# Kernel tuning notes

Hardware: AMD Instinct MI355X
Metric: run time of the kernel (lower is better)

## Reference

```python
import jax, jax.numpy as jnp
import numpy as np

B, S, E, H = 4, 4096, 1024, 16
D = E // H  # head_dim = 64
EPS = 1e-6


def setup_inputs() -> dict:
    key = jax.random.key(0)
    ks = jax.random.split(key, 11)
    inv = 1.0 / np.sqrt(E)
    return {
        "query": jax.random.normal(ks[0], (B, S, E), dtype=jnp.float32),
        "key": jax.random.normal(ks[1], (B, S, E), dtype=jnp.float32),
        "value": jax.random.normal(ks[2], (B, S, E), dtype=jnp.float32),
        "key_padding_mask": jnp.zeros((B, S), dtype=bool),
        "Wq": jax.random.uniform(ks[3], (E, E), jnp.float32, -inv, inv),
        "bq": jnp.zeros((E,), jnp.float32),
        "Wk": jax.random.uniform(ks[4], (E, E), jnp.float32, -inv, inv),
        "bk": jnp.zeros((E,), jnp.float32),
        "Wv": jax.random.uniform(ks[5], (E, E), jnp.float32, -inv, inv),
        "bv": jnp.zeros((E,), jnp.float32),
        "Wo": jax.random.uniform(ks[6], (E, E), jnp.float32, -inv, inv),
        "bo": jnp.zeros((E,), jnp.float32),
    }


def _heads(x):
    # (B,S,E) -> (B,H,S,D)
    return x.reshape(B, -1, H, D).transpose(0, 2, 1, 3)


def reference(query, key, value, key_padding_mask, Wq, bq, Wk, bk, Wv, bv, Wo, bo):
    q = _heads(query @ Wq.T + bq)
    k = _heads(key @ Wk.T + bk)
    v = _heads(value @ Wv.T + bv)

    q_aug = jax.nn.relu(q) + EPS
    k_aug = jax.nn.relu(k) + EPS
    # mask out padded keys: (B,S_k) -> (B,1,S_k,1)
    k_aug = jnp.where(key_padding_mask[:, None, :, None], 0.0, k_aug)

    kv_context = jnp.einsum("bhsd,bhsv->bhdv", k_aug, v)  # (B,H,D,D)
    k_sum = k_aug.sum(axis=2)                                # (B,H,D)
    denom = jnp.einsum("bhqd,bhd->bhq", q_aug, k_sum)
    denom = jnp.maximum(denom, EPS)

    attn = jnp.einsum("bhqd,bhdv->bhqv", q_aug, kv_context) / denom[..., None]
    attn = attn.transpose(0, 2, 1, 3).reshape(B, -1, E)      # (B,S_q,E)
    # dropout is identity in eval mode
    return attn @ Wo.T + bo
```

## Files before the change

kernel.cpp:

```cpp
#include <hip/hip_runtime.h>
#include <hip/hip_bf16.h>
#include <stdint.h>

#define B_ 4
#define S_ 4096
#define E_ 1024
#define H_ 16
#define D_ 64
#define M_ (B_*S_)
constexpr float kEPS = 1e-6f;

typedef unsigned short u16;
typedef unsigned char  u8;
typedef __bf16 bf16x8 __attribute__((ext_vector_type(8)));
typedef float  f32x4  __attribute__((ext_vector_type(4)));
typedef u16    u16x8  __attribute__((ext_vector_type(8)));

typedef const __attribute__((address_space(1))) void* gaddr_t;
typedef __attribute__((address_space(3))) void*       laddr_t;

__device__ __forceinline__ u16 f2bf(float f) {
    union { float f; uint32_t u; } v; v.f = f;
    uint32_t u = v.u;
    u += 0x7fffu + ((u >> 16) & 1u);
    return (u16)(u >> 16);
}
__device__ __forceinline__ float hi2f(uint32_t d) {
    union { uint32_t u; float f; } v; v.u = d & 0xffff0000u;
    return v.f;
}
__device__ __forceinline__ float lo2f(uint32_t d) {
    union { uint32_t u; float f; } v; v.u = d << 16;
    return v.f;
}

#define VM_WAIT(n) asm volatile("s_waitcnt vmcnt(" #n ")" ::: "memory")
#define LG0        asm volatile("s_waitcnt lgkmcnt(0)" ::: "memory")
#define SBAR       asm volatile("s_barrier" ::: "memory")

__global__ __launch_bounds__(256)
void cvt3_kernel(const float* __restrict__ s0, const float* __restrict__ s1,
                 const float* __restrict__ s2,
                 u16* __restrict__ d0, u16* __restrict__ d1, u16* __restrict__ d2,
                 int n4)
{
    const int z = blockIdx.y;
    const float* src = (z == 0) ? s0 : (z == 1) ? s1 : s2;
    u16*         dst = (z == 0) ? d0 : (z == 1) ? d1 : d2;
    const int stride = gridDim.x * blockDim.x;
    for (int i = blockIdx.x * blockDim.x + threadIdx.x; i < n4; i += stride) {
        float4 v = reinterpret_cast<const float4*>(src)[i];
        ushort4 o;
        o.x = f2bf(v.x); o.y = f2bf(v.y); o.z = f2bf(v.z); o.w = f2bf(v.w);
        reinterpret_cast<ushort4*>(dst)[i] = o;
    }
}

__global__ __launch_bounds__(256)
void cvtw_kernel(const float* __restrict__ w0, const float* __restrict__ w1,
                 const float* __restrict__ w2, const float* __restrict__ w3,
                 u16* __restrict__ o0, u16* __restrict__ o1,
                 u16* __restrict__ o2, u16* __restrict__ o3)
{
    const int z = blockIdx.y;
    const float* src = (z == 0) ? w0 : (z == 1) ? w1 : (z == 2) ? w2 : w3;
    u16*         dst = (z == 0) ? o0 : (z == 1) ? o1 : (z == 2) ? o2 : o3;
    const int i = blockIdx.x * blockDim.x + threadIdx.x;
    float4 v = reinterpret_cast<const float4*>(src)[i];
    ushort4 o;
    o.x = f2bf(v.x); o.y = f2bf(v.y); o.z = f2bf(v.z); o.w = f2bf(v.w);
    reinterpret_cast<ushort4*>(dst)[i] = o;
}

#define BM 256
#define BN 256
#define BKT 64
#define NKT (E_/BKT)

struct QKVArgs {
    const u16*   A[3];
    const u16*   W[3];
    const float* bias[3];
    const u8*    mask;
    u16*         C[3];
};

template<bool MERGED>
__global__ __launch_bounds__(512, 2)
void gemm8(QKVArgs qa,
           const u16* __restrict__ A1, const u16* __restrict__ Bw1,
           const float* __restrict__ bias1, float* __restrict__ Cf)
{
    extern __shared__ u16 lds[];
    const int tid  = threadIdx.x;
    const int wid  = tid >> 6, lane = tid & 63;
    const int wqr  = wid >> 2, wqc = wid & 3;
    const int m0   = blockIdx.x * BM;
    const int n0   = blockIdx.y * BN;
    const int fr   = lane & 15;
    const int cg   = lane >> 4;

    const u16* A;  const u16* Bw;  const float* bias;  u16* Cb;  int epi;
    if constexpr (MERGED) {
        const int z = blockIdx.z;
        A = qa.A[z]; Bw = qa.W[z]; bias = qa.bias[z]; Cb = qa.C[z]; epi = z + 1;
    } else {
        A = A1; Bw = Bw1; bias = bias1; Cb = nullptr; epi = 0;
    }

    const int srow = tid >> 3;
    const int ssc  = tid & 7;
    const int sck  = ssc ^ (srow & 7);
    const u16* aS = A  + (size_t)(m0 + srow)*E_ + sck*8;
    const u16* bS = Bw + (size_t)(n0 + srow)*E_ + sck*8;
    const int sd0 = tid*8, sd1 = (tid + 512)*8;

    int arow[4], brow[2];
#pragma unroll
    for (int mf = 0; mf < 4; ++mf) arow[mf] = (wqr*64 + mf*16 + fr) * 64;
#pragma unroll
    for (int nf = 0; nf < 2; ++nf) brow[nf] = (wqc*32 + nf*16 + fr) * 64;
    const int kx0 = ((cg)     ^ (fr & 7)) * 8;
    const int kx1 = ((4 + cg) ^ (fr & 7)) * 8;

    f32x4 acc[2][2][4][2] = {};
    bf16x8 afr[4][2];

    float bias_v[2][2];
#pragma unroll
    for (int nh = 0; nh < 2; ++nh)
#pragma unroll
        for (int nf = 0; nf < 2; ++nf)
            bias_v[nh][nf] = bias[n0 + nh*128 + wqc*32 + nf*16 + fr];

#define STAGE(BUF, MAT, HH, T) do { \
        u16* dst_ = lds + (BUF)*32768 + (MAT)*16384 + (HH)*8192; \
        const u16* src_ = ((MAT) ? bS : aS) + (size_t)(HH)*128*E_ + (size_t)(T)*BKT; \
        __builtin_amdgcn_global_load_lds((gaddr_t)(src_),                  (laddr_t)(dst_ + sd0), 16, 0, 0); \
        __builtin_amdgcn_global_load_lds((gaddr_t)(src_ + (size_t)64*E_), (laddr_t)(dst_ + sd1), 16, 0, 0); \
    } while (0)

#define PH(BUF, MH, NH, STG_STMT, WAIT_STMT) do { \
        const u16* Ab_ = lds + (BUF)*32768 + (MH)*8192; \
        const u16* Bb_ = lds + (BUF)*32768 + 16384 + (NH)*8192; \
        if ((NH) == 0) { \
            _Pragma("unroll") \
            for (int mf_ = 0; mf_ < 4; ++mf_) { \
                afr[mf_][0] = *reinterpret_cast<const bf16x8*>(Ab_ + arow[mf_] + kx0); \
                afr[mf_][1] = *reinterpret_cast<const bf16x8*>(Ab_ + arow[mf_] + kx1); \
            } \
        } \
        bf16x8 bfv[2][2]; \
        _Pragma("unroll") \
        for (int nf_ = 0; nf_ < 2; ++nf_) { \
            bfv[nf_][0] = *reinterpret_cast<const bf16x8*>(Bb_ + brow[nf_] + kx0); \
            bfv[nf_][1] = *reinterpret_cast<const bf16x8*>(Bb_ + brow[nf_] + kx1); \
        } \
        STG_STMT; \
        WAIT_STMT; \
        SBAR; \
        LG0; \
        __builtin_amdgcn_sched_barrier(0); \
        __builtin_amdgcn_s_setprio(1); \
        _Pragma("unroll") \
        for (int mf_ = 0; mf_ < 4; ++mf_) { \
            _Pragma("unroll") \
            for (int nf_ = 0; nf_ < 2; ++nf_) { \
                acc[MH][NH][mf_][nf_] = __builtin_amdgcn_mfma_f32_16x16x32_bf16(afr[mf_][0], bfv[nf_][0], acc[MH][NH][mf_][nf_], 0, 0, 0); \
                acc[MH][NH][mf_][nf_] = __builtin_amdgcn_mfma_f32_16x16x32_bf16(afr[mf_][1], bfv[nf_][1], acc[MH][NH][mf_][nf_], 0, 0, 0); \
            } \
        } \
        __builtin_amdgcn_s_setprio(0); \
        SBAR; \
    } while (0)

    STAGE(0, 0, 0, 0);
    STAGE(0, 1, 0, 0);
    STAGE(0, 0, 1, 0);
    STAGE(0, 1, 1, 0);
    STAGE(1, 0, 0, 1);
    STAGE(1, 1, 0, 1);
    VM_WAIT(4);
    SBAR;
    __builtin_amdgcn_sched_barrier(0);

#pragma unroll 1
    for (int i = 0; i < 7; ++i) {
        const int T1 = 2*i + 1, T2 = 2*i + 2, T3 = 2*i + 3;
        PH(0, 0, 0, STAGE(1, 0, 1, T1), ;);
        PH(0, 0, 1, STAGE(1, 1, 1, T1), ;);
        PH(0, 1, 0, STAGE(0, 0, 0, T2), ;);
        PH(0, 1, 1, STAGE(0, 1, 0, T2), VM_WAIT(4));
        PH(1, 0, 0, STAGE(0, 0, 1, T2), ;);
        PH(1, 0, 1, STAGE(0, 1, 1, T2), ;);
        PH(1, 1, 0, STAGE(1, 0, 0, T3), ;);
        PH(1, 1, 1, STAGE(1, 1, 0, T3), VM_WAIT(4));
    }
    PH(0, 0, 0, STAGE(1, 0, 1, 15), ;);
    PH(0, 0, 1, STAGE(1, 1, 1, 15), ;);
    PH(0, 1, 0, ;, ;);
    PH(0, 1, 1, ;, VM_WAIT(0));
    PH(1, 0, 0, ;, ;);
    PH(1, 0, 1, ;, ;);
    PH(1, 1, 0, ;, ;);
    PH(1, 1, 1, ;, ;);
#undef PH
#undef STAGE

    const int bblk = m0 >> 12;
    const int sloc = m0 & 4095;
#pragma unroll
    for (int mh = 0; mh < 2; ++mh) {
#pragma unroll
    for (int nh = 0; nh < 2; ++nh) {
#pragma unroll
    for (int mf = 0; mf < 4; ++mf) {
#pragma unroll
        for (int nf = 0; nf < 2; ++nf) {
            const int gn = n0 + nh*128 + wqc*32 + nf*16 + fr;
            const int mb = mh*128 + wqr*64 + mf*16 + cg*4;
            if (epi >= 2) {
                ushort4 o;
#pragma unroll
                for (int r = 0; r < 4; ++r) {
                    float x = acc[mh][nh][mf][nf][r] + bias_v[nh][nf];
                    if (epi == 2) {
                        x = fmaxf(x, 0.f) + kEPS;
                        if (qa.mask[m0 + mb + r]) x = 0.f;
                    }
                    ((u16*)&o)[r] = f2bf(x);
                }
                *reinterpret_cast<ushort4*>(Cb + ((size_t)(bblk*1024 + gn))*4096 + sloc + mb) = o;
            } else if (epi == 1) {
#pragma unroll
                for (int r = 0; r < 4; ++r) {
                    const int gm = m0 + mb + r;
                    float x = acc[mh][nh][mf][nf][r] + bias_v[nh][nf];
                    x = fmaxf(x, 0.f) + kEPS;
                    Cb[(size_t)gm*E_ + gn] = f2bf(x);
                }
            } else {
#pragma unroll
                for (int r = 0; r < 4; ++r) {
                    const int gm = m0 + mb + r;
                    Cf[(size_t)gm*E_ + gn] = acc[mh][nh][mf][nf][r] + bias_v[nh][nf];
                }
            }
        }
    }
    }
    }
}

#define NSC 8
#define KCH (S_/NSC)
__global__ __launch_bounds__(256)
void kv_mfma_kernel(const u16* __restrict__ KaT, const u16* __restrict__ VvT,
                    float* __restrict__ kvp, float* __restrict__ ksp)
{
    __shared__ float sm[4][64];
    const int bh = blockIdx.x, sc = blockIdx.y;
    const int tid = threadIdx.x;
    const int w = tid >> 6, lane = tid & 63;
    const int fr = lane & 15, cg = lane >> 4;

    const u16* Ar = VvT + ((size_t)bh*64 + w*16 + fr)*4096 + sc*KCH;
    const u16* Br0 = KaT + ((size_t)bh*64 + fr)*4096 + sc*KCH;

    f32x4 acc[4] = {};
#pragma unroll 2
    for (int ks = 0; ks < KCH/32; ++ks) {
        const int ko = ks*32 + cg*8;
        bf16x8 af = *reinterpret_cast<const bf16x8*>(Ar + ko);
#pragma unroll
        for (int nf = 0; nf < 4; ++nf) {
            bf16x8 bf = *reinterpret_cast<const bf16x8*>(Br0 + (size_t)nf*16*4096 + ko);
            acc[nf] = __builtin_amdgcn_mfma_f32_16x16x32_bf16(af, bf, acc[nf], 0, 0, 0);
        }
    }
    float* dst = kvp + ((size_t)sc*64 + bh)*4096;
#pragma unroll
    for (int nf = 0; nf < 4; ++nf)
#pragma unroll
        for (int r = 0; r < 4; ++r)
            dst[(w*16 + cg*4 + r)*64 + nf*16 + fr] = acc[nf][r];

    {
        const int d = tid & 63, qq = tid >> 6;
        const u16* kr = KaT + ((size_t)bh*64 + d)*4096 + sc*KCH + qq*(KCH/4);
        float s = 0.f;
#pragma unroll 4
        for (int i = 0; i < KCH/4/8; ++i) {
            bf16x8 kk = *reinterpret_cast<const bf16x8*>(kr + i*8);
#pragma unroll
            for (int j = 0; j < 8; ++j) s += (float)kk[j];
        }
        sm[qq][d] = s;
    }
    __syncthreads();
    if (tid < 64)
        ksp[((size_t)sc*64 + bh)*64 + tid] = sm[0][tid] + sm[1][tid] + sm[2][tid] + sm[3][tid];
}

__global__ __launch_bounds__(256)
void kv_reduce_kernel(const float* __restrict__ kvp, const float* __restrict__ ksp,
                      u16* __restrict__ kvT, float* __restrict__ ksum)
{
    const int i = blockIdx.x*256 + threadIdx.x;
    float s = 0.f;
#pragma unroll
    for (int c = 0; c < NSC; ++c) s += kvp[(size_t)c*262144 + i];
    kvT[i] = f2bf(s);
    if (i < 4096) {
        float t = 0.f;
#pragma unroll
        for (int c = 0; c < NSC; ++c) t += ksp[(size_t)c*4096 + i];
        ksum[i] = t;
    }
}

__global__ __launch_bounds__(256)
void attn_kernel(const u16* __restrict__ Qa, const u16* __restrict__ kvT,
                 const float* __restrict__ ksum, u16* __restrict__ attn)
{
    __shared__ u16  Qs[256*64];
    __shared__ u16  Ts[64*64];
    __shared__ float kss[64];
    __shared__ float invd[256];

    const int bh = blockIdx.x, b = bh >> 4, h = bh & 15;
    const int s0 = blockIdx.y * 256;
    const int tid = threadIdx.x;
    const int wid = tid >> 6, lane = tid & 63;
    const int fr = lane & 15, cg = lane >> 4;

#pragma unroll
    for (int j = 0; j < 8; ++j) {
        int L = (wid*8 + j)*64 + lane;
        int row = L >> 3, c = L & 7;
        int cs = c ^ (row & 7);
        const u16* src = Qa + (size_t)(b*S_ + s0 + row)*E_ + h*64 + cs*8;
        __builtin_amdgcn_global_load_lds((gaddr_t)src, (laddr_t)(Qs + L*8), 16, 0, 0);
    }
#pragma unroll
    for (int k = 0; k < 2; ++k) {
        int g = k*256 + tid;
        int v = g >> 3, c = g & 7;
        uint4 q = *reinterpret_cast<const uint4*>(kvT + (size_t)bh*4096 + g*8);
        int cs = c ^ (v & 7);
        *reinterpret_cast<uint4*>(Ts + v*64 + cs*8) = q;
    }
    if (tid < 64) kss[tid] = ksum[bh*64 + tid];
    asm volatile("s_waitcnt vmcnt(0) lgkmcnt(0)" ::: "memory");
    __syncthreads();

    {
        float den = 0.f;
#pragma unroll
        for (int c = 0; c < 8; ++c) {
            uint4 qc = *reinterpret_cast<const uint4*>(Qs + tid*64 + (c ^ (tid & 7))*8);
            den += lo2f(qc.x)*kss[c*8+0] + hi2f(qc.x)*kss[c*8+1]
                 + lo2f(qc.y)*kss[c*8+2] + hi2f(qc.y)*kss[c*8+3]
                 + lo2f(qc.z)*kss[c*8+4] + hi2f(qc.z)*kss[c*8+5]
                 + lo2f(qc.w)*kss[c*8+6] + hi2f(qc.w)*kss[c*8+7];
        }
        invd[tid] = 1.0f / fmaxf(den, kEPS);
    }
    __syncthreads();

    f32x4 acc[4][4] = {};
#pragma unroll
    for (int ks = 0; ks < 2; ++ks) {
        bf16x8 bfrag[4];
#pragma unroll
        for (int nf = 0; nf < 4; ++nf) {
            int v = nf*16 + fr;
            bfrag[nf] = *reinterpret_cast<const bf16x8*>(Ts + v*64 + ((ks*4 + cg) ^ (v & 7))*8);
        }
#pragma unroll
        for (int mf = 0; mf < 4; ++mf) {
            int m = wid*64 + mf*16 + fr;
            bf16x8 afrag = *reinterpret_cast<const bf16x8*>(Qs + m*64 + ((ks*4 + cg) ^ (m & 7))*8);
#pragma unroll
            for (int nf = 0; nf < 4; ++nf)
                acc[mf][nf] = __builtin_amdgcn_mfma_f32_16x16x32_bf16(afrag, bfrag[nf], acc[mf][nf], 0, 0, 0);
        }
    }

#pragma unroll
    for (int mf = 0; mf < 4; ++mf) {
#pragma unroll
        for (int nf = 0; nf < 4; ++nf) {
            const int v = nf*16 + fr;
#pragma unroll
            for (int r = 0; r < 4; ++r) {
                const int row = wid*64 + mf*16 + cg*4 + r;
                float x = acc[mf][nf][r] * invd[row];
                attn[(size_t)(b*S_ + s0 + row)*E_ + h*64 + v] = f2bf(x);
            }
        }
    }
}

extern "C" void kernel_launch(void* const* d_in, const int* in_sizes, int n_in,
                              void* d_out, int out_size, void* d_ws, size_t ws_size,
                              hipStream_t stream)
{
    const float* query = (const float*)d_in[0];
    const float* key   = (const float*)d_in[1];
    const float* value = (const float*)d_in[2];
    const u8*    mask  = (const u8*)d_in[3];
    const float* Wq = (const float*)d_in[4];
    const float* bq = (const float*)d_in[5];
    const float* Wk = (const float*)d_in[6];
    const float* bk = (const float*)d_in[7];
    const float* Wv = (const float*)d_in[8];
    const float* bv = (const float*)d_in[9];
    const float* Wo = (const float*)d_in[10];
    const float* bo = (const float*)d_in[11];
    float* out = (float*)d_out;

    const size_t SZ_ME = (size_t)M_ * E_;
    const size_t SZ_EE = (size_t)E_ * E_;

    char* ws = (char*)d_ws;
    u16* qx   = (u16*)ws; ws += SZ_ME*2;
    u16* kx   = (u16*)ws; ws += SZ_ME*2;
    u16* vx   = (u16*)ws; ws += SZ_ME*2;
    u16* Qa   = (u16*)ws; ws += SZ_ME*2;
    u16* KaT  = (u16*)ws; ws += SZ_ME*2;
    u16* VvT  = (u16*)ws; ws += SZ_ME*2;
    u16* wqb  = (u16*)ws; ws += SZ_EE*2;
    u16* wkb  = (u16*)ws; ws += SZ_EE*2;
    u16* wvb  = (u16*)ws; ws += SZ_EE*2;
    u16* wob  = (u16*)ws; ws += SZ_EE*2;
    float* kvp = (float*)ws; ws += (size_t)NSC*64*4096*4;
    float* ksp = (float*)ws; ws += (size_t)NSC*4096*4;
    u16*  kvT  = (u16*)ws;  ws += (size_t)64*4096*2;
    float* ksum= (float*)ws; ws += 4096*4;

    u16* attnb = qx;

    cvt3_kernel<<<dim3(2048, 3), 256, 0, stream>>>(query, key, value, qx, kx, vx, (int)(SZ_ME/4));
    cvtw_kernel<<<dim3(1024, 4), 256, 0, stream>>>(Wq, Wk, Wv, Wo, wqb, wkb, wvb, wob);

    QKVArgs qa;
    qa.A[0] = qx;  qa.A[1] = kx;  qa.A[2] = vx;
    qa.W[0] = wqb; qa.W[1] = wkb; qa.W[2] = wvb;
    qa.bias[0] = bq; qa.bias[1] = bk; qa.bias[2] = bv;
    qa.mask = mask;
    qa.C[0] = Qa; qa.C[1] = KaT; qa.C[2] = VvT;
    dim3 ggrid(M_/BM, E_/BN, 3);
    constexpr size_t LDS_BYTES = 2 * 32768 * sizeof(u16);
    gemm8<true><<<ggrid, 512, LDS_BYTES, stream>>>(qa, nullptr, nullptr, nullptr, nullptr);

    kv_mfma_kernel<<<dim3(64, NSC), 256, 0, stream>>>(KaT, VvT, kvp, ksp);
    kv_reduce_kernel<<<1024, 256, 0, stream>>>(kvp, ksp, kvT, ksum);

    attn_kernel<<<dim3(B_*H_, S_/256), 256, 0, stream>>>(Qa, kvT, ksum, attnb);

    QKVArgs dummy = {};
    dummy.mask = mask;
    gemm8<false><<<dim3(M_/BM, E_/BN, 1), 512, LDS_BYTES, stream>>>(dummy, attnb, wob, bo, out);
}
```

Baseline: 263.8 us.

## Reuse B fragments across M halves and deepen GEMM prefetch to full stage

The GEMM main loop now keeps two B-fragment register sets and loads B from LDS only once per N-half, reusing it across both M-halves, which cuts LDS reads. The stage ordering and vmcnt waits are reworked so a full next K-tile is prefetched with finer-grained waits that allow more global loads in flight. This adds register pressure and makes the wait counts delicate, so a miscount could create a race or a stall.

```diff
diff --git a/kernel.cpp b/kernel.cpp
--- a/kernel.cpp
+++ b/kernel.cpp
@@ -125,6 +125,7 @@
 
     f32x4 acc[2][2][4][2] = {};
     bf16x8 afr[4][2];
+    bf16x8 bfr0[2][2], bfr1[2][2];
 
     float bias_v[2][2];
 #pragma unroll
@@ -140,21 +141,22 @@
         __builtin_amdgcn_global_load_lds((gaddr_t)(src_ + (size_t)64*E_), (laddr_t)(dst_ + sd1), 16, 0, 0); \
     } while (0)
 
-#define PH(BUF, MH, NH, STG_STMT, WAIT_STMT) do { \
-        const u16* Ab_ = lds + (BUF)*32768 + (MH)*8192; \
-        const u16* Bb_ = lds + (BUF)*32768 + 16384 + (NH)*8192; \
-        if ((NH) == 0) { \
+#define PH(BUF, MH, NH, BFRX, LOADA, LOADB, STG_STMT, WAIT_STMT) do { \
+        if (LOADA) { \
+            const u16* Ab_ = lds + (BUF)*32768 + (MH)*8192; \
             _Pragma("unroll") \
             for (int mf_ = 0; mf_ < 4; ++mf_) { \
                 afr[mf_][0] = *reinterpret_cast<const bf16x8*>(Ab_ + arow[mf_] + kx0); \
                 afr[mf_][1] = *reinterpret_cast<const bf16x8*>(Ab_ + arow[mf_] + kx1); \
             } \
         } \
-        bf16x8 bfv[2][2]; \
-        _Pragma("unroll") \
-        for (int nf_ = 0; nf_ < 2; ++nf_) { \
-            bfv[nf_][0] = *reinterpret_cast<const bf16x8*>(Bb_ + brow[nf_] + kx0); \
-            bfv[nf_][1] = *reinterpret_cast<const bf16x8*>(Bb_ + brow[nf_] + kx1); \
+        if (LOADB) { \
+            const u16* Bb_ = lds + (BUF)*32768 + 16384 + (NH)*8192; \
+            _Pragma("unroll") \
+            for (int nf_ = 0; nf_ < 2; ++nf_) { \
+                BFRX[nf_][0] = *reinterpret_cast<const bf16x8*>(Bb_ + brow[nf_] + kx0); \
+                BFRX[nf_][1] = *reinterpret_cast<const bf16x8*>(Bb_ + brow[nf_] + kx1); \
+            } \
         } \
         STG_STMT; \
         WAIT_STMT; \
@@ -166,44 +168,44 @@
         for (int mf_ = 0; mf_ < 4; ++mf_) { \
             _Pragma("unroll") \
             for (int nf_ = 0; nf_ < 2; ++nf_) { \
-                acc[MH][NH][mf_][nf_] = __builtin_amdgcn_mfma_f32_16x16x32_bf16(afr[mf_][0], bfv[nf_][0], acc[MH][NH][mf_][nf_], 0, 0, 0); \
-                acc[MH][NH][mf_][nf_] = __builtin_amdgcn_mfma_f32_16x16x32_bf16(afr[mf_][1], bfv[nf_][1], acc[MH][NH][mf_][nf_], 0, 0, 0); \
+                acc[MH][NH][mf_][nf_] = __builtin_amdgcn_mfma_f32_16x16x32_bf16(afr[mf_][0], BFRX[nf_][0], acc[MH][NH][mf_][nf_], 0, 0, 0); \
+                acc[MH][NH][mf_][nf_] = __builtin_amdgcn_mfma_f32_16x16x32_bf16(afr[mf_][1], BFRX[nf_][1], acc[MH][NH][mf_][nf_], 0, 0, 0); \
             } \
         } \
         __builtin_amdgcn_s_setprio(0); \
         SBAR; \
     } while (0)
 
-    STAGE(0, 0, 0, 0);
-    STAGE(0, 1, 0, 0);
+    STAGE(0, 0, 0, 0); STAGE(0, 1, 0, 0);
+    STAGE(0, 1, 1, 0);
     STAGE(0, 0, 1, 0);
-    STAGE(0, 1, 1, 0);
-    STAGE(1, 0, 0, 1);
-    STAGE(1, 1, 0, 1);
-    VM_WAIT(4);
+    STAGE(1, 0, 0, 1); STAGE(1, 1, 0, 1);
+    STAGE(1, 1, 1, 1);
+    STAGE(1, 0, 1, 1);
+    VM_WAIT(8);
     SBAR;
     __builtin_amdgcn_sched_barrier(0);
 
 #pragma unroll 1
     for (int i = 0; i < 7; ++i) {
-        const int T1 = 2*i + 1, T2 = 2*i + 2, T3 = 2*i + 3;
-        PH(0, 0, 0, STAGE(1, 0, 1, T1), ;);
-        PH(0, 0, 1, STAGE(1, 1, 1, T1), ;);
-        PH(0, 1, 0, STAGE(0, 0, 0, T2), ;);
-        PH(0, 1, 1, STAGE(0, 1, 0, T2), VM_WAIT(4));
-        PH(1, 0, 0, STAGE(0, 0, 1, T2), ;);
-        PH(1, 0, 1, STAGE(0, 1, 1, T2), ;);
-        PH(1, 1, 0, STAGE(1, 0, 0, T3), ;);
-        PH(1, 1, 1, STAGE(1, 1, 0, T3), VM_WAIT(4));
-    }
-    PH(0, 0, 0, STAGE(1, 0, 1, 15), ;);
-    PH(0, 0, 1, STAGE(1, 1, 1, 15), ;);
-    PH(0, 1, 0, ;, ;);
-    PH(0, 1, 1, ;, VM_WAIT(0));
-    PH(1, 0, 0, ;, ;);
-    PH(1, 0, 1, ;, ;);
-    PH(1, 1, 0, ;, ;);
-    PH(1, 1, 1, ;, ;);
+        const int T2 = 2*i + 2, T3 = 2*i + 3;
+        PH(0, 0, 0, bfr0, 1, 1, ;,                                        VM_WAIT(10));
+        PH(0, 0, 1, bfr1, 0, 1, { STAGE(0,0,0,T2); STAGE(0,1,0,T2); },    VM_WAIT(12));
+        PH(0, 1, 0, bfr0, 1, 0, STAGE(0,1,1,T2),                          ;);
+        PH(0, 1, 1, bfr1, 0, 0, STAGE(0,0,1,T2),                          VM_WAIT(12));
+        PH(1, 0, 0, bfr0, 1, 1, ;,                                        VM_WAIT(10));
+        PH(1, 0, 1, bfr1, 0, 1, { STAGE(1,0,0,T3); STAGE(1,1,0,T3); },    VM_WAIT(12));
+        PH(1, 1, 0, bfr0, 1, 0, STAGE(1,1,1,T3),                          ;);
+        PH(1, 1, 1, bfr1, 0, 0, STAGE(1,0,1,T3),                          VM_WAIT(12));
+    }
+    PH(0, 0, 0, bfr0, 1, 1, ;, VM_WAIT(10));
+    PH(0, 0, 1, bfr1, 0, 1, ;, VM_WAIT(8));
+    PH(0, 1, 0, bfr0, 1, 0, ;, ;);
+    PH(0, 1, 1, bfr1, 0, 0, ;, VM_WAIT(4));
+    PH(1, 0, 0, bfr0, 1, 1, ;, VM_WAIT(2));
+    PH(1, 0, 1, bfr1, 0, 1, ;, VM_WAIT(0));
+    PH(1, 1, 0, bfr0, 1, 0, ;, ;);
+    PH(1, 1, 1, bfr1, 0, 0, ;, ;);
 #undef PH
 #undef STAGE
 
```

After: 261.5 us, median of 2. Within noise of the previous version (-0.9%).

## Replace 256x256 eight-phase GEMM with simpler 256x128 double-buffered kernel

Applied to the files above, without the earlier changes.

The hand-scheduled 256x256x64 GEMM with its eight-phase quarter-tile pipeline is replaced by a 256x128 tile with K-step 32 and a plain double-buffered loop that prefetches the next K slice while issuing MFMAs on the current one. The LDS footprint drops, and launch bounds now ask for four blocks per CU, aiming at higher occupancy and more blocks in the grid. In exchange, each tile reuses its operands less and takes a full barrier plus vmcnt(0) wait on every K step, so more global/L2 traffic and more synchronisation overhead are exposed. The LDS swizzle is rewritten for the 32-wide K slice.

```diff
diff --git a/kernel.cpp b/kernel.cpp
--- a/kernel.cpp
+++ b/kernel.cpp
@@ -72,10 +72,10 @@
     reinterpret_cast<ushort4*>(dst)[i] = o;
 }
 
-#define BM 256
-#define BN 256
-#define BKT 64
-#define NKT (E_/BKT)
+#define BM2 256
+#define BN2 128
+#define BKT2 32
+#define NT2 (E_/BKT2)
 
 struct QKVArgs {
     const u16*   A[3];
@@ -86,17 +86,17 @@
 };
 
 template<bool MERGED>
-__global__ __launch_bounds__(512, 2)
-void gemm8(QKVArgs qa,
-           const u16* __restrict__ A1, const u16* __restrict__ Bw1,
-           const float* __restrict__ bias1, float* __restrict__ Cf)
+__global__ __launch_bounds__(512, 4)
+void gemm2b(QKVArgs qa,
+            const u16* __restrict__ A1, const u16* __restrict__ Bw1,
+            const float* __restrict__ bias1, float* __restrict__ Cf)
 {
     extern __shared__ u16 lds[];
     const int tid  = threadIdx.x;
     const int wid  = tid >> 6, lane = tid & 63;
-    const int wqr  = wid >> 2, wqc = wid & 3;
-    const int m0   = blockIdx.x * BM;
-    const int n0   = blockIdx.y * BN;
+    const int wqr  = wid >> 1, wqc = wid & 1;
+    const int m0   = blockIdx.x * BM2;
+    const int n0   = blockIdx.y * BN2;
     const int fr   = lane & 15;
     const int cg   = lane >> 4;
 
@@ -108,122 +108,78 @@
         A = A1; Bw = Bw1; bias = bias1; Cb = nullptr; epi = 0;
     }
 
-    const int srow = tid >> 3;
-    const int ssc  = tid & 7;
-    const int sck  = ssc ^ (srow & 7);
-    const u16* aS = A  + (size_t)(m0 + srow)*E_ + sck*8;
-    const u16* bS = Bw + (size_t)(n0 + srow)*E_ + sck*8;
-    const int sd0 = tid*8, sd1 = (tid + 512)*8;
-
-    int arow[4], brow[2];
-#pragma unroll
-    for (int mf = 0; mf < 4; ++mf) arow[mf] = (wqr*64 + mf*16 + fr) * 64;
-#pragma unroll
-    for (int nf = 0; nf < 2; ++nf) brow[nf] = (wqc*32 + nf*16 + fr) * 64;
-    const int kx0 = ((cg)     ^ (fr & 7)) * 8;
-    const int kx1 = ((4 + cg) ^ (fr & 7)) * 8;
-
-    f32x4 acc[2][2][4][2] = {};
-    bf16x8 afr[4][2];
-
-    float bias_v[2][2];
-#pragma unroll
-    for (int nh = 0; nh < 2; ++nh)
-#pragma unroll
-        for (int nf = 0; nf < 2; ++nf)
-            bias_v[nh][nf] = bias[n0 + nh*128 + wqc*32 + nf*16 + fr];
-
-#define STAGE(BUF, MAT, HH, T) do { \
-        u16* dst_ = lds + (BUF)*32768 + (MAT)*16384 + (HH)*8192; \
-        const u16* src_ = ((MAT) ? bS : aS) + (size_t)(HH)*128*E_ + (size_t)(T)*BKT; \
-        __builtin_amdgcn_global_load_lds((gaddr_t)(src_),                  (laddr_t)(dst_ + sd0), 16, 0, 0); \
-        __builtin_amdgcn_global_load_lds((gaddr_t)(src_ + (size_t)64*E_), (laddr_t)(dst_ + sd1), 16, 0, 0); \
+    const int srow = tid >> 2;
+    const int skey = (srow ^ (srow >> 2)) & 3;
+    const int sck  = (tid & 3) ^ skey;
+    const u16* aS0 = A  + (size_t)(m0 + srow)*E_        + sck*8;
+    const u16* aS1 = A  + (size_t)(m0 + 128 + srow)*E_  + sck*8;
+    const u16* bS0 = Bw + (size_t)(n0 + srow)*E_        + sck*8;
+
+    const int lkey = (fr ^ (fr >> 2)) & 3;
+    const int kxr  = (cg ^ lkey) * 8;
+    int arow[4], brow[4];
+#pragma unroll
+    for (int mf = 0; mf < 4; ++mf) arow[mf] = (wqr*64 + mf*16 + fr)*32 + kxr;
+#pragma unroll
+    for (int nf = 0; nf < 4; ++nf) brow[nf] = 8192 + (wqc*64 + nf*16 + fr)*32 + kxr;
+
+    f32x4 acc[4][4] = {};
+
+    float bias_v[4];
+#pragma unroll
+    for (int nf = 0; nf < 4; ++nf) bias_v[nf] = bias[n0 + wqc*64 + nf*16 + fr];
+
+#define STAGE(BUF, T) do { \
+        const size_t ko_ = (size_t)(T) * BKT2; \
+        u16* ab_ = lds + (BUF)*12288; \
+        __builtin_amdgcn_global_load_lds((gaddr_t)(aS0 + ko_), (laddr_t)(ab_ + tid*8),          16, 0, 0); \
+        __builtin_amdgcn_global_load_lds((gaddr_t)(aS1 + ko_), (laddr_t)(ab_ + (tid+512)*8),    16, 0, 0); \
+        __builtin_amdgcn_global_load_lds((gaddr_t)(bS0 + ko_), (laddr_t)(ab_ + 8192 + tid*8),   16, 0, 0); \
     } while (0)
 
-#define PH(BUF, MH, NH, STG_STMT, WAIT_STMT) do { \
-        const u16* Ab_ = lds + (BUF)*32768 + (MH)*8192; \
-        const u16* Bb_ = lds + (BUF)*32768 + 16384 + (NH)*8192; \
-        if ((NH) == 0) { \
-            _Pragma("unroll") \
-            for (int mf_ = 0; mf_ < 4; ++mf_) { \
-                afr[mf_][0] = *reinterpret_cast<const bf16x8*>(Ab_ + arow[mf_] + kx0); \
-                afr[mf_][1] = *reinterpret_cast<const bf16x8*>(Ab_ + arow[mf_] + kx1); \
-            } \
-        } \
-        bf16x8 bfv[2][2]; \
-        _Pragma("unroll") \
-        for (int nf_ = 0; nf_ < 2; ++nf_) { \
-            bfv[nf_][0] = *reinterpret_cast<const bf16x8*>(Bb_ + brow[nf_] + kx0); \
-            bfv[nf_][1] = *reinterpret_cast<const bf16x8*>(Bb_ + brow[nf_] + kx1); \
-        } \
-        STG_STMT; \
-        WAIT_STMT; \
-        SBAR; \
-        LG0; \
-        __builtin_amdgcn_sched_barrier(0); \
-        __builtin_amdgcn_s_setprio(1); \
-        _Pragma("unroll") \
-        for (int mf_ = 0; mf_ < 4; ++mf_) { \
-            _Pragma("unroll") \
-            for (int nf_ = 0; nf_ < 2; ++nf_) { \
-                acc[MH][NH][mf_][nf_] = __builtin_amdgcn_mfma_f32_16x16x32_bf16(afr[mf_][0], bfv[nf_][0], acc[MH][NH][mf_][nf_], 0, 0, 0); \
-                acc[MH][NH][mf_][nf_] = __builtin_amdgcn_mfma_f32_16x16x32_bf16(afr[mf_][1], bfv[nf_][1], acc[MH][NH][mf_][nf_], 0, 0, 0); \
-            } \
-        } \
-        __builtin_amdgcn_s_setprio(0); \
-        SBAR; \
-    } while (0)
-
-    STAGE(0, 0, 0, 0);
-    STAGE(0, 1, 0, 0);
-    STAGE(0, 0, 1, 0);
-    STAGE(0, 1, 1, 0);
-    STAGE(1, 0, 0, 1);
-    STAGE(1, 1, 0, 1);
-    VM_WAIT(4);
+    STAGE(0, 0);
+    VM_WAIT(0);
     SBAR;
     __builtin_amdgcn_sched_barrier(0);
 
 #pragma unroll 1
-    for (int i = 0; i < 7; ++i) {
-        const int T1 = 2*i + 1, T2 = 2*i + 2, T3 = 2*i + 3;
-        PH(0, 0, 0, STAGE(1, 0, 1, T1), ;);
-        PH(0, 0, 1, STAGE(1, 1, 1, T1), ;);
-        PH(0, 1, 0, STAGE(0, 0, 0, T2), ;);
-        PH(0, 1, 1, STAGE(0, 1, 0, T2), VM_WAIT(4));
-        PH(1, 0, 0, STAGE(0, 0, 1, T2), ;);
-        PH(1, 0, 1, STAGE(0, 1, 1, T2), ;);
-        PH(1, 1, 0, STAGE(1, 0, 0, T3), ;);
-        PH(1, 1, 1, STAGE(1, 1, 0, T3), VM_WAIT(4));
-    }
-    PH(0, 0, 0, STAGE(1, 0, 1, 15), ;);
-    PH(0, 0, 1, STAGE(1, 1, 1, 15), ;);
-    PH(0, 1, 0, ;, ;);
-    PH(0, 1, 1, ;, VM_WAIT(0));
-    PH(1, 0, 0, ;, ;);
-    PH(1, 0, 1, ;, ;);
-    PH(1, 1, 0, ;, ;);
-    PH(1, 1, 1, ;, ;);
-#undef PH
+    for (int T = 0; T < NT2; ++T) {
+        const int cb = T & 1;
+        const u16* buf = lds + cb*12288;
+        bf16x8 afr[4], bfv[4];
+#pragma unroll
+        for (int mf = 0; mf < 4; ++mf) afr[mf] = *reinterpret_cast<const bf16x8*>(buf + arow[mf]);
+#pragma unroll
+        for (int nf = 0; nf < 4; ++nf) bfv[nf] = *reinterpret_cast<const bf16x8*>(buf + brow[nf]);
+        if (T < NT2 - 1) STAGE(cb ^ 1, T + 1);
+        LG0;
+        __builtin_amdgcn_sched_barrier(0);
+        __builtin_amdgcn_s_setprio(1);
+#pragma unroll
+        for (int mf = 0; mf < 4; ++mf)
+#pragma unroll
+            for (int nf = 0; nf < 4; ++nf)
+                acc[mf][nf] = __builtin_amdgcn_mfma_f32_16x16x32_bf16(afr[mf], bfv[nf], acc[mf][nf], 0, 0, 0);
+        __builtin_amdgcn_s_setprio(0);
+        VM_WAIT(0);
+        SBAR;
+        __builtin_amdgcn_sched_barrier(0);
+    }
 #undef STAGE
 
     const int bblk = m0 >> 12;
     const int sloc = m0 & 4095;
 #pragma unroll
-    for (int mh = 0; mh < 2; ++mh) {
-#pragma unroll
-    for (int nh = 0; nh < 2; ++nh) {
-#pragma unroll
     for (int mf = 0; mf < 4; ++mf) {
 #pragma unroll
-        for (int nf = 0; nf < 2; ++nf) {
-            const int gn = n0 + nh*128 + wqc*32 + nf*16 + fr;
-            const int mb = mh*128 + wqr*64 + mf*16 + cg*4;
+        for (int nf = 0; nf < 4; ++nf) {
+            const int gn = n0 + wqc*64 + nf*16 + fr;
+            const int mb = wqr*64 + mf*16 + cg*4;
             if (epi >= 2) {
                 ushort4 o;
 #pragma unroll
                 for (int r = 0; r < 4; ++r) {
-                    float x = acc[mh][nh][mf][nf][r] + bias_v[nh][nf];
+                    float x = acc[mf][nf][r] + bias_v[nf];
                     if (epi == 2) {
                         x = fmaxf(x, 0.f) + kEPS;
                         if (qa.mask[m0 + mb + r]) x = 0.f;
@@ -235,7 +191,7 @@
 #pragma unroll
                 for (int r = 0; r < 4; ++r) {
                     const int gm = m0 + mb + r;
-                    float x = acc[mh][nh][mf][nf][r] + bias_v[nh][nf];
+                    float x = acc[mf][nf][r] + bias_v[nf];
                     x = fmaxf(x, 0.f) + kEPS;
                     Cb[(size_t)gm*E_ + gn] = f2bf(x);
                 }
@@ -243,12 +199,10 @@
 #pragma unroll
                 for (int r = 0; r < 4; ++r) {
                     const int gm = m0 + mb + r;
-                    Cf[(size_t)gm*E_ + gn] = acc[mh][nh][mf][nf][r] + bias_v[nh][nf];
+                    Cf[(size_t)gm*E_ + gn] = acc[mf][nf][r] + bias_v[nf];
                 }
             }
         }
-    }
-    }
     }
 }
 
@@ -450,9 +404,9 @@
     qa.bias[0] = bq; qa.bias[1] = bk; qa.bias[2] = bv;
     qa.mask = mask;
     qa.C[0] = Qa; qa.C[1] = KaT; qa.C[2] = VvT;
-    dim3 ggrid(M_/BM, E_/BN, 3);
-    constexpr size_t LDS_BYTES = 2 * 32768 * sizeof(u16);
-    gemm8<true><<<ggrid, 512, LDS_BYTES, stream>>>(qa, nullptr, nullptr, nullptr, nullptr);
+    dim3 ggrid(M_/BM2, E_/BN2, 3);
+    constexpr size_t LDS_BYTES = 2 * 12288 * sizeof(u16);
+    gemm2b<true><<<ggrid, 512, LDS_BYTES, stream>>>(qa, nullptr, nullptr, nullptr, nullptr);
 
     kv_mfma_kernel<<<dim3(64, NSC), 256, 0, stream>>>(KaT, VvT, kvp, ksp);
     kv_reduce_kernel<<<1024, 256, 0, stream>>>(kvp, ksp, kvT, ksum);
@@ -461,5 +415,5 @@
 
     QKVArgs dummy = {};
     dummy.mask = mask;
-    gemm8<false><<<dim3(M_/BM, E_/BN, 1), 512, LDS_BYTES, stream>>>(dummy, attnb, wob, bo, out);
-}
+    gemm2b<false><<<dim3(M_/BM2, E_/BN2, 1), 512, LDS_BYTES, stream>>>(dummy, attnb, wob, bo, out);
+}
```

Measured after the change: 279.9 us. 1.06x slower.

## Make QKV GEMM persistent over three projections with cross-GEMM prefetch

Applied to the files above, without the earlier changes.

Replaces the z-dimension grid of three projection GEMMs with a single block that processes Q, K and V sequentially for the same tile. The next projection's first k-tiles are staged into LDS during the tail of the current one, so pipeline fill and epilogue overlap across projections. This also removes the wave-quantization tail of the larger grid and preloads mask bytes as packed words. In exchange the grid launches only one block per CU, so occupancy is halved, and register pressure rises from holding three bias sets.

```diff
diff --git a/kernel.cpp b/kernel.cpp
--- a/kernel.cpp
+++ b/kernel.cpp
@@ -85,11 +85,11 @@
     u16*         C[3];
 };
 
-template<bool MERGED>
+template<int NZ>
 __global__ __launch_bounds__(512, 2)
-void gemm8(QKVArgs qa,
-           const u16* __restrict__ A1, const u16* __restrict__ Bw1,
-           const float* __restrict__ bias1, float* __restrict__ Cf)
+void gemm8z(QKVArgs qa,
+            const u16* __restrict__ A1, const u16* __restrict__ Bw1,
+            const float* __restrict__ bias1, float* __restrict__ Cf)
 {
     extern __shared__ u16 lds[];
     const int tid  = threadIdx.x;
@@ -100,19 +100,11 @@
     const int fr   = lane & 15;
     const int cg   = lane >> 4;
 
-    const u16* A;  const u16* Bw;  const float* bias;  u16* Cb;  int epi;
-    if constexpr (MERGED) {
-        const int z = blockIdx.z;
-        A = qa.A[z]; Bw = qa.W[z]; bias = qa.bias[z]; Cb = qa.C[z]; epi = z + 1;
-    } else {
-        A = A1; Bw = Bw1; bias = bias1; Cb = nullptr; epi = 0;
-    }
-
     const int srow = tid >> 3;
     const int ssc  = tid & 7;
     const int sck  = ssc ^ (srow & 7);
-    const u16* aS = A  + (size_t)(m0 + srow)*E_ + sck*8;
-    const u16* bS = Bw + (size_t)(n0 + srow)*E_ + sck*8;
+    const size_t aofs = (size_t)(m0 + srow)*E_ + sck*8;
+    const size_t bofs = (size_t)(n0 + srow)*E_ + sck*8;
     const int sd0 = tid*8, sd1 = (tid + 512)*8;
 
     int arow[4], brow[2];
@@ -126,19 +118,40 @@
     f32x4 acc[2][2][4][2] = {};
     bf16x8 afr[4][2];
 
-    float bias_v[2][2];
-#pragma unroll
-    for (int nh = 0; nh < 2; ++nh)
-#pragma unroll
-        for (int nf = 0; nf < 2; ++nf)
-            bias_v[nh][nf] = bias[n0 + nh*128 + wqc*32 + nf*16 + fr];
-
-#define STAGE(BUF, MAT, HH, T) do { \
+    float ba[NZ][2][2];
+#pragma unroll
+    for (int j = 0; j < NZ; ++j) {
+        const float* bp = (NZ == 3)
+            ? ((j == 0) ? qa.bias[0] : (j == 1) ? qa.bias[1] : qa.bias[2])
+            : bias1;
+#pragma unroll
+        for (int nh = 0; nh < 2; ++nh)
+#pragma unroll
+            for (int nf = 0; nf < 2; ++nf)
+                ba[j][nh][nf] = bp[n0 + nh*128 + wqc*32 + nf*16 + fr];
+    }
+    uint32_t mask_w[8] = {};
+    if constexpr (NZ == 3) {
+#pragma unroll
+        for (int mh = 0; mh < 2; ++mh)
+#pragma unroll
+            for (int mf = 0; mf < 4; ++mf)
+                mask_w[mh*4+mf] = *reinterpret_cast<const uint32_t*>(
+                    qa.mask + m0 + mh*128 + wqr*64 + mf*16 + cg*4);
+    }
+
+    const u16* Acur = (NZ == 3) ? qa.A[0] : A1;
+    const u16* Bcur = (NZ == 3) ? qa.W[0] : Bw1;
+
+#define STG(AP, BP, BUF, MAT, HH, T) do { \
         u16* dst_ = lds + (BUF)*32768 + (MAT)*16384 + (HH)*8192; \
-        const u16* src_ = ((MAT) ? bS : aS) + (size_t)(HH)*128*E_ + (size_t)(T)*BKT; \
+        const u16* src_ = ((MAT) ? ((BP) + bofs) : ((AP) + aofs)) \
+                          + (size_t)(HH)*128*E_ + (size_t)(T)*BKT; \
         __builtin_amdgcn_global_load_lds((gaddr_t)(src_),                  (laddr_t)(dst_ + sd0), 16, 0, 0); \
         __builtin_amdgcn_global_load_lds((gaddr_t)(src_ + (size_t)64*E_), (laddr_t)(dst_ + sd1), 16, 0, 0); \
     } while (0)
+#define STAGE(BUF, MAT, HH, T)  STG(Acur,  Bcur,  BUF, MAT, HH, T)
+#define STAGEN(BUF, MAT, HH, T) STG(Anext, Bnext, BUF, MAT, HH, T)
 
 #define PH(BUF, MH, NH, STG_STMT, WAIT_STMT) do { \
         const u16* Ab_ = lds + (BUF)*32768 + (MH)*8192; \
@@ -185,71 +198,121 @@
     __builtin_amdgcn_sched_barrier(0);
 
 #pragma unroll 1
-    for (int i = 0; i < 7; ++i) {
-        const int T1 = 2*i + 1, T2 = 2*i + 2, T3 = 2*i + 3;
-        PH(0, 0, 0, STAGE(1, 0, 1, T1), ;);
-        PH(0, 0, 1, STAGE(1, 1, 1, T1), ;);
-        PH(0, 1, 0, STAGE(0, 0, 0, T2), ;);
-        PH(0, 1, 1, STAGE(0, 1, 0, T2), VM_WAIT(4));
-        PH(1, 0, 0, STAGE(0, 0, 1, T2), ;);
-        PH(1, 0, 1, STAGE(0, 1, 1, T2), ;);
-        PH(1, 1, 0, STAGE(1, 0, 0, T3), ;);
-        PH(1, 1, 1, STAGE(1, 1, 0, T3), VM_WAIT(4));
-    }
-    PH(0, 0, 0, STAGE(1, 0, 1, 15), ;);
-    PH(0, 0, 1, STAGE(1, 1, 1, 15), ;);
-    PH(0, 1, 0, ;, ;);
-    PH(0, 1, 1, ;, VM_WAIT(0));
-    PH(1, 0, 0, ;, ;);
-    PH(1, 0, 1, ;, ;);
-    PH(1, 1, 0, ;, ;);
-    PH(1, 1, 1, ;, ;);
+    for (int z = 0; z < NZ; ++z) {
+        const u16* Anext = Acur;
+        const u16* Bnext = Bcur;
+        if constexpr (NZ == 3) {
+            Anext = (z == 0) ? qa.A[1] : qa.A[2];
+            Bnext = (z == 0) ? qa.W[1] : qa.W[2];
+        }
+
+#pragma unroll 1
+        for (int i = 0; i < 7; ++i) {
+            const int T1 = 2*i + 1, T2 = 2*i + 2, T3 = 2*i + 3;
+            PH(0, 0, 0, STAGE(1, 0, 1, T1), ;);
+            PH(0, 0, 1, STAGE(1, 1, 1, T1), ;);
+            PH(0, 1, 0, STAGE(0, 0, 0, T2), ;);
+            PH(0, 1, 1, STAGE(0, 1, 0, T2), VM_WAIT(4));
+            PH(1, 0, 0, STAGE(0, 0, 1, T2), ;);
+            PH(1, 0, 1, STAGE(0, 1, 1, T2), ;);
+            PH(1, 1, 0, STAGE(1, 0, 0, T3), ;);
+            PH(1, 1, 1, STAGE(1, 1, 0, T3), VM_WAIT(4));
+        }
+        if (z < NZ - 1) {
+            PH(0, 0, 0, STAGE(1, 0, 1, 15), ;);
+            PH(0, 0, 1, STAGE(1, 1, 1, 15), ;);
+            PH(0, 1, 0, STAGEN(0, 0, 0, 0), ;);
+            PH(0, 1, 1, STAGEN(0, 1, 0, 0), VM_WAIT(4));
+            PH(1, 0, 0, STAGEN(0, 0, 1, 0), ;);
+            PH(1, 0, 1, STAGEN(0, 1, 1, 0), ;);
+            PH(1, 1, 0, STAGEN(1, 0, 0, 1), ;);
+            PH(1, 1, 1, STAGEN(1, 1, 0, 1), VM_WAIT(4));
+        } else {
+            PH(0, 0, 0, STAGE(1, 0, 1, 15), ;);
+            PH(0, 0, 1, STAGE(1, 1, 1, 15), ;);
+            PH(0, 1, 0, ;, ;);
+            PH(0, 1, 1, ;, VM_WAIT(0));
+            PH(1, 0, 0, ;, ;);
+            PH(1, 0, 1, ;, ;);
+            PH(1, 1, 0, ;, ;);
+            PH(1, 1, 1, ;, ;);
+        }
+
+        const int epi = (NZ == 3) ? z + 1 : 0;
+        u16* Cb = nullptr;
+        if constexpr (NZ == 3)
+            Cb = (z == 0) ? qa.C[0] : (z == 1) ? qa.C[1] : qa.C[2];
+        float bcur[2][2];
+#pragma unroll
+        for (int nh = 0; nh < 2; ++nh)
+#pragma unroll
+            for (int nf = 0; nf < 2; ++nf)
+                bcur[nh][nf] = (NZ == 1 || z == 0) ? ba[0][nh][nf]
+                             : (NZ == 3 && z == 1) ? ba[NZ > 1 ? 1 : 0][nh][nf]
+                                                   : ba[NZ > 2 ? 2 : 0][nh][nf];
+
+        const int bblk = m0 >> 12;
+        const int sloc = m0 & 4095;
+#pragma unroll
+        for (int mh = 0; mh < 2; ++mh) {
+#pragma unroll
+        for (int nh = 0; nh < 2; ++nh) {
+#pragma unroll
+        for (int mf = 0; mf < 4; ++mf) {
+#pragma unroll
+            for (int nf = 0; nf < 2; ++nf) {
+                const int gn = n0 + nh*128 + wqc*32 + nf*16 + fr;
+                const int mb = mh*128 + wqr*64 + mf*16 + cg*4;
+                if (epi >= 2) {
+                    ushort4 o;
+#pragma unroll
+                    for (int r = 0; r < 4; ++r) {
+                        float x = acc[mh][nh][mf][nf][r] + bcur[nh][nf];
+                        if (epi == 2) {
+                            x = fmaxf(x, 0.f) + kEPS;
+                            if ((mask_w[mh*4+mf] >> (r*8)) & 0xffu) x = 0.f;
+                        }
+                        ((u16*)&o)[r] = f2bf(x);
+                    }
+                    *reinterpret_cast<ushort4*>(Cb + ((size_t)(bblk*1024 + gn))*4096 + sloc + mb) = o;
+                } else if (epi == 1) {
+#pragma unroll
+                    for (int r = 0; r < 4; ++r) {
+                        const int gm = m0 + mb + r;
+                        float x = acc[mh][nh][mf][nf][r] + bcur[nh][nf];
+                        x = fmaxf(x, 0.f) + kEPS;
+                        Cb[(size_t)gm*E_ + gn] = f2bf(x);
+                    }
+                } else {
+#pragma unroll
+                    for (int r = 0; r < 4; ++r) {
+                        const int gm = m0 + mb + r;
+                        Cf[(size_t)gm*E_ + gn] = acc[mh][nh][mf][nf][r] + bcur[nh][nf];
+                    }
+                }
+            }
+        }
+        }
+        }
+
+        if (z < NZ - 1) {
+#pragma unroll
+            for (int a = 0; a < 2; ++a)
+#pragma unroll
+            for (int b = 0; b < 2; ++b)
+#pragma unroll
+            for (int c = 0; c < 4; ++c)
+#pragma unroll
+            for (int d = 0; d < 2; ++d)
+                acc[a][b][c][d] = f32x4{0.f, 0.f, 0.f, 0.f};
+            Acur = Anext;
+            Bcur = Bnext;
+        }
+    }
 #undef PH
 #undef STAGE
-
-    const int bblk = m0 >> 12;
-    const int sloc = m0 & 4095;
-#pragma unroll
-    for (int mh = 0; mh < 2; ++mh) {
-#pragma unroll
-    for (int nh = 0; nh < 2; ++nh) {
-#pragma unroll
-    for (int mf = 0; mf < 4; ++mf) {
-#pragma unroll
-        for (int nf = 0; nf < 2; ++nf) {
-            const int gn = n0 + nh*128 + wqc*32 + nf*16 + fr;
-            const int mb = mh*128 + wqr*64 + mf*16 + cg*4;
-            if (epi >= 2) {
-                ushort4 o;
-#pragma unroll
-                for (int r = 0; r < 4; ++r) {
-                    float x = acc[mh][nh][mf][nf][r] + bias_v[nh][nf];
-                    if (epi == 2) {
-                        x = fmaxf(x, 0.f) + kEPS;
-                        if (qa.mask[m0 + mb + r]) x = 0.f;
-                    }
-                    ((u16*)&o)[r] = f2bf(x);
-                }
-                *reinterpret_cast<ushort4*>(Cb + ((size_t)(bblk*1024 + gn))*4096 + sloc + mb) = o;
-            } else if (epi == 1) {
-#pragma unroll
-                for (int r = 0; r < 4; ++r) {
-                    const int gm = m0 + mb + r;
-                    float x = acc[mh][nh][mf][nf][r] + bias_v[nh][nf];
-                    x = fmaxf(x, 0.f) + kEPS;
-                    Cb[(size_t)gm*E_ + gn] = f2bf(x);
-                }
-            } else {
-#pragma unroll
-                for (int r = 0; r < 4; ++r) {
-                    const int gm = m0 + mb + r;
-                    Cf[(size_t)gm*E_ + gn] = acc[mh][nh][mf][nf][r] + bias_v[nh][nf];
-                }
-            }
-        }
-    }
-    }
-    }
+#undef STAGEN
+#undef STG
 }
 
 #define NSC 8
@@ -450,9 +513,8 @@
     qa.bias[0] = bq; qa.bias[1] = bk; qa.bias[2] = bv;
     qa.mask = mask;
     qa.C[0] = Qa; qa.C[1] = KaT; qa.C[2] = VvT;
-    dim3 ggrid(M_/BM, E_/BN, 3);
     constexpr size_t LDS_BYTES = 2 * 32768 * sizeof(u16);
-    gemm8<true><<<ggrid, 512, LDS_BYTES, stream>>>(qa, nullptr, nullptr, nullptr, nullptr);
+    gemm8z<3><<<dim3(M_/BM, E_/BN), 512, LDS_BYTES, stream>>>(qa, nullptr, nullptr, nullptr, nullptr);
 
     kv_mfma_kernel<<<dim3(64, NSC), 256, 0, stream>>>(KaT, VvT, kvp, ksp);
     kv_reduce_kernel<<<1024, 256, 0, stream>>>(kvp, ksp, kvT, ksum);
@@ -461,5 +523,5 @@
 
     QKVArgs dummy = {};
     dummy.mask = mask;
-    gemm8<false><<<dim3(M_/BM, E_/BN, 1), 512, LDS_BYTES, stream>>>(dummy, attnb, wob, bo, out);
-}
+    gemm8z<1><<<dim3(M_/BM, E_/BN), 512, LDS_BYTES, stream>>>(dummy, attnb, wob, bo, out);
+}
```

New measurement: 495.1 us. +87.7%, slower.
